# Performance work log

Hardware: AMD Instinct MI355X
Metric: run time of the kernel (lower is better)

Reference implementation:

```python
import jax, jax.numpy as jnp
import numpy as np

B, S, D, H, E, K = 2, 1024, 1024, 4096, 8, 2
HE = 4 * D  # expert FFN inner dim
LN_EPS = 1e-5


def layernorm(x, g, b):
    m = x.mean(-1, keepdims=True)
    v = ((x - m) ** 2).mean(-1, keepdims=True)
    return (x - m) * jax.lax.rsqrt(v + LN_EPS) * g + b


def pos_encoding(S, D):
    pos = jnp.arange(S, dtype=jnp.float32)[:, None]
    i = jnp.arange(0, D, 2, dtype=jnp.float32)
    div = jnp.exp(-(jnp.log(10000.0)) * i / D)
    pe = jnp.zeros((S, D), dtype=jnp.float32)
    pe = pe.at[:, 0::2].set(jnp.sin(pos * div))
    pe = pe.at[:, 1::2].set(jnp.cos(pos * div))
    return pe


def setup_inputs() -> dict:
    key = jax.random.key(0)
    ks = jax.random.split(key, 16)
    w = lambda k, sh, s=0.02: (jax.random.normal(k, sh, dtype=jnp.float32) * s)
    return {
        "x": jax.random.normal(ks[0], (B, S, D), dtype=jnp.float32),
        # router: LayerNorm -> Linear(D,H) -> GELU -> Linear(H,E)
        "r_ln_g": jnp.ones((D,), jnp.float32), "r_ln_b": jnp.zeros((D,), jnp.float32),
        "r_w1": w(ks[1], (D, H)), "r_b1": jnp.zeros((H,), jnp.float32),
        "r_w2": w(ks[2], (H, E)), "r_b2": jnp.zeros((E,), jnp.float32),
        "temperature": jnp.ones((1,), jnp.float32) * 0.07,
        # stacked expert params: LayerNorm -> Linear(D,HE) -> GELU -> Linear(HE,D)
        "e_ln_g": jnp.ones((E, D), jnp.float32), "e_ln_b": jnp.zeros((E, D), jnp.float32),
        "e_w1": w(ks[3], (E, D, HE)), "e_b1": jnp.zeros((E, HE), jnp.float32),
        "e_w2": w(ks[4], (E, HE, D)), "e_b2": jnp.zeros((E, D), jnp.float32),
        # combiner: LayerNorm -> Linear(D,2D) -> GELU -> Linear(2D,D)
        "c_ln_g": jnp.ones((D,), jnp.float32), "c_ln_b": jnp.zeros((D,), jnp.float32),
        "c_w1": w(ks[5], (D, 2 * D)), "c_b1": jnp.zeros((2 * D,), jnp.float32),
        "c_w2": w(ks[6], (2 * D, D)), "c_b2": jnp.zeros((D,), jnp.float32),
        "o_ln_g": jnp.ones((D,), jnp.float32), "o_ln_b": jnp.zeros((D,), jnp.float32),
    }


def reference(x, r_ln_g, r_ln_b, r_w1, r_b1, r_w2, r_b2, temperature,
              e_ln_g, e_ln_b, e_w1, e_b1, e_w2, e_b2,
              c_ln_g, c_ln_b, c_w1, c_b1, c_w2, c_b2, o_ln_g, o_ln_b):
    gelu = lambda t: jax.nn.gelu(t, approximate=False)
    h = x + pos_encoding(S, D)[None]  # [B,S,D]
    # router logits with learned temperature
    r = layernorm(h, r_ln_g, r_ln_b)
    r = gelu(jnp.einsum("bsd,dh->bsh", r, r_w1) + r_b1)
    logits = (jnp.einsum("bsh,he->bse", r, r_w2) + r_b2) / temperature
    probs = jax.nn.softmax(logits, axis=-1)  # [B,S,E]
    topk_p, topk_i = jax.lax.top_k(probs, K)
    # sparse gate [B,S,E]: softmax prob on selected experts, 0 elsewhere
    gate = (jax.nn.one_hot(topk_i, E, dtype=probs.dtype) * topk_p[..., None]).sum(-2)
    # per-expert FFN on all tokens (dense reference of dispatch/compute/combine)
    m = h.mean(-1, keepdims=True)
    v = ((h - m) ** 2).mean(-1, keepdims=True)
    xhat = (h - m) * jax.lax.rsqrt(v + LN_EPS)  # [B,S,D], shared LN stats
    y = xhat[None] * e_ln_g[:, None, None, :] + e_ln_b[:, None, None, :]  # [E,B,S,D]
    f = gelu(jnp.einsum("ebsd,edh->ebsh", y, e_w1) + e_b1[:, None, None, :])
    f = jnp.einsum("ebsh,ehd->ebsd", f, e_w2) + e_b2[:, None, None, :]
    combined = jnp.einsum("bse,ebsd->bsd", gate, f)
    # expert combiner MLP + residual + output norm
    c = layernorm(combined, c_ln_g, c_ln_b)
    c = gelu(jnp.einsum("bsd,de->bse", c, c_w1) + c_b1)
    c = jnp.einsum("bse,ed->bsd", c, c_w2) + c_b2
    return layernorm(h + c, o_ln_g, o_ln_b)
```

## Files before the change

### kernel.cpp

```cpp
#include <hip/hip_runtime.h>
#include <stdint.h>

#define TOK 2048
#define DD  1024
#define RH  4096
#define HE  4096
#define NE  8
#define CH  2048
#define MAXTILE 40
#define MAXROWS 5120
#define KSG2 4
#define KSC1 2
#define KSC2 4

using bf16x8 = __attribute__((ext_vector_type(8))) short;
using f32x4  = __attribute__((ext_vector_type(4))) float;

__device__ __forceinline__ unsigned short f2bf(float f) {
  union { float f; uint32_t u; } v; v.f = f;
  uint32_t r = (v.u + 0x7fffu + ((v.u >> 16) & 1u)) >> 16;
  return (unsigned short)r;
}
__device__ __forceinline__ float bf2f(unsigned short h) {
  union { uint32_t u; float f; } v; v.u = ((uint32_t)h) << 16;
  return v.f;
}
__device__ __forceinline__ float gelu_f(float x) {
  return 0.5f * x * (1.0f + erff(x * 0.70710678118654752440f));
}

#define GLD(SRC, DST) __builtin_amdgcn_global_load_lds( \
    (const __attribute__((address_space(1))) uint32_t*)(const void*)(SRC), \
    (__attribute__((address_space(3))) uint32_t*)(void*)(DST), 16, 0, 0)

__device__ __forceinline__ void block_ln_stats(float s1, float s2, float& mean, float& rstd) {
  #pragma unroll
  for (int off = 32; off > 0; off >>= 1) {
    s1 += __shfl_down(s1, off);
    s2 += __shfl_down(s2, off);
  }
  __shared__ float sh[8];
  int tid = threadIdx.x;
  if ((tid & 63) == 0) { sh[tid >> 6] = s1; sh[4 + (tid >> 6)] = s2; }
  __syncthreads();
  float t1 = sh[0] + sh[1] + sh[2] + sh[3];
  float t2 = sh[4] + sh[5] + sh[6] + sh[7];
  mean = t1 * (1.0f / 1024.0f);
  float var = t2 * (1.0f / 1024.0f) - mean * mean;
  rstd = rsqrtf(var + 1e-5f);
}

__global__ void k_prep(const float* __restrict__ x, float* __restrict__ h,
                       float* __restrict__ xh32, unsigned short* __restrict__ xhi,
                       unsigned short* __restrict__ xlo) {
  int t = blockIdx.x;
  int s = t & 1023;
  int tid = threadIdx.x;
  float4 xv = ((const float4*)(x + (size_t)t * DD))[tid];
  float v[4]; float s1 = 0.f, s2 = 0.f;
  #pragma unroll
  for (int k = 0; k < 4; ++k) {
    int d = tid * 4 + k;
    float xc = (k == 0) ? xv.x : (k == 1) ? xv.y : (k == 2) ? xv.z : xv.w;
    float i2 = (float)(d & ~1);
    float div = expf(-9.2103403719761836f * i2 * (1.0f / 1024.0f));
    float ang = (float)s * div;
    float pe = (d & 1) ? cosf(ang) : sinf(ang);
    float hv = xc + pe;
    v[k] = hv; s1 += hv; s2 += hv * hv;
  }
  float mean, rstd;
  block_ln_stats(s1, s2, mean, rstd);
  float4 ho; ho.x = v[0]; ho.y = v[1]; ho.z = v[2]; ho.w = v[3];
  ((float4*)(h + (size_t)t * DD))[tid] = ho;
  float xn[4]; unsigned short hh[4], ll[4];
  #pragma unroll
  for (int k = 0; k < 4; ++k) {
    xn[k] = (v[k] - mean) * rstd;
    hh[k] = f2bf(xn[k]);
    ll[k] = f2bf(xn[k] - bf2f(hh[k]));
  }
  float4 xo; xo.x = xn[0]; xo.y = xn[1]; xo.z = xn[2]; xo.w = xn[3];
  ((float4*)(xh32 + (size_t)t * DD))[tid] = xo;
  ushort4 h4; h4.x = hh[0]; h4.y = hh[1]; h4.z = hh[2]; h4.w = hh[3];
  ((ushort4*)(xhi + (size_t)t * DD))[tid] = h4;
  ushort4 l4; l4.x = ll[0]; l4.y = ll[1]; l4.z = ll[2]; l4.w = ll[3];
  ((ushort4*)(xlo + (size_t)t * DD))[tid] = l4;
}

__global__ void k_tconv(const float* __restrict__ in, const float* __restrict__ g,
                        unsigned short* __restrict__ out, int D, int N,
                        long long in_bs, long long g_bs, long long out_bs) {
  __shared__ float tile[64][65];
  int e = blockIdx.z;
  const float* inb = in + (size_t)e * in_bs;
  unsigned short* outb = out + (size_t)e * out_bs;
  int n0 = blockIdx.x * 64, d0 = blockIdx.y * 64;
  int c4 = threadIdx.x & 15;
  int r0 = threadIdx.x >> 4;
  #pragma unroll
  for (int rr = 0; rr < 4; ++rr) {
    int dl = r0 + rr * 16;
    float4 v = *(const float4*)(inb + (size_t)(d0 + dl) * N + n0 + c4 * 4);
    if (g) {
      float gv = g[(size_t)e * g_bs + d0 + dl];
      v.x *= gv; v.y *= gv; v.z *= gv; v.w *= gv;
    }
    tile[dl][c4 * 4 + 0] = v.x; tile[dl][c4 * 4 + 1] = v.y;
    tile[dl][c4 * 4 + 2] = v.z; tile[dl][c4 * 4 + 3] = v.w;
  }
  __syncthreads();
  int q = threadIdx.x & 15;
  int nb = threadIdx.x >> 4;
  #pragma unroll
  for (int rr = 0; rr < 4; ++rr) {
    int nl = nb + rr * 16;
    ushort4 o;
    o.x = f2bf(tile[q * 4 + 0][nl]); o.y = f2bf(tile[q * 4 + 1][nl]);
    o.z = f2bf(tile[q * 4 + 2][nl]); o.w = f2bf(tile[q * 4 + 3][nl]);
    *(ushort4*)(outb + (size_t)(n0 + nl) * D + d0 + q * 4) = o;
  }
}

__global__ void k_tconv_split(const float* __restrict__ in, const float* __restrict__ g,
                              unsigned short* __restrict__ oh, unsigned short* __restrict__ ol,
                              float* __restrict__ o32, int D, int N) {
  __shared__ float tile[32][33];
  int n0 = blockIdx.x * 32, d0 = blockIdx.y * 32;
  int tn = threadIdx.x & 31, tr = threadIdx.x >> 5;
  #pragma unroll
  for (int rr = 0; rr < 4; ++rr) {
    int dl = tr + rr * 8;
    float v = in[(size_t)(d0 + dl) * N + n0 + tn];
    if (g) v *= g[d0 + dl];
    tile[dl][tn] = v;
  }
  __syncthreads();
  #pragma unroll
  for (int rr = 0; rr < 4; ++rr) {
    int nl = tr + rr * 8;
    float v = tile[tn][nl];
    size_t off = (size_t)(n0 + nl) * D + d0 + tn;
    unsigned short hi = f2bf(v);
    oh[off] = hi;
    ol[off] = f2bf(v - bf2f(hi));
    o32[off] = v;
  }
}

__global__ void k_foldbias(const float* __restrict__ w, const float* __restrict__ lnb,
                           const float* __restrict__ b1, float* __restrict__ outb,
                           int D, int N, long long w_bs, long long lnb_bs,
                           long long b_bs, long long o_bs) {
  int e = blockIdx.y;
  int n = blockIdx.x * 256 + threadIdx.x;
  const float* wb = w + (size_t)e * w_bs;
  const float* lb = lnb + (size_t)e * lnb_bs;
  float acc = b1[(size_t)e * b_bs + n];
  for (int d = 0; d < D; ++d) {
    float l = lb[d];
    if (l != 0.f) acc += l * wb[(size_t)d * N + n];
  }
  outb[(size_t)e * o_bs + n] = acc;
}

__global__ __launch_bounds__(256)
void k_gemm_sk(const unsigned short* __restrict__ A, const unsigned short* __restrict__ B,
               float* __restrict__ C, int N, int K, int kslice, long long c_slice) {
  __shared__ __align__(16) unsigned short As[128 * 32];
  __shared__ __align__(16) unsigned short Bs[128 * 32];
  const int tid = threadIdx.x;
  const int w = tid >> 6, lane = tid & 63;
  const int q = lane >> 4, r16 = lane & 15;
  const int kz = blockIdx.z;
  const int n0 = blockIdx.x * 128, m0 = blockIdx.y * 128;
  f32x4 acc[4][4];
  #pragma unroll
  for (int i = 0; i < 4; ++i)
    #pragma unroll
    for (int j = 0; j < 4; ++j) acc[i][j] = (f32x4){0.f, 0.f, 0.f, 0.f};
  const int srow = w * 32 + (lane >> 2);
  const int scol = (lane & 3) * 8;
  const unsigned short* a_src = A + (size_t)(m0 + srow) * K + scol + (size_t)kz * kslice;
  const unsigned short* b_src = B + (size_t)(n0 + srow) * K + scol + (size_t)kz * kslice;
  unsigned short* a_dst = &As[w * 1024];
  unsigned short* b_dst = &Bs[w * 1024];
  const int wm = w >> 1, wn = w & 1;
  for (int kt = 0; kt < kslice; kt += 32) {
    GLD(a_src + kt, a_dst);
    GLD(a_src + kt + (size_t)16 * K, a_dst + 512);
    GLD(b_src + kt, b_dst);
    GLD(b_src + kt + (size_t)16 * K, b_dst + 512);
    __syncthreads();
    bf16x8 af[4], bfv[4];
    #pragma unroll
    for (int i = 0; i < 4; ++i)
      af[i] = *(const bf16x8*)&As[(wm * 64 + i * 16 + r16) * 32 + q * 8];
    #pragma unroll
    for (int j = 0; j < 4; ++j)
      bfv[j] = *(const bf16x8*)&Bs[(wn * 64 + j * 16 + r16) * 32 + q * 8];
    #pragma unroll
    for (int i = 0; i < 4; ++i)
      #pragma unroll
      for (int j = 0; j < 4; ++j)
        acc[i][j] = __builtin_amdgcn_mfma_f32_16x16x32_bf16(af[i], bfv[j], acc[i][j], 0, 0, 0);
    __syncthreads();
  }
  #pragma unroll
  for (int j = 0; j < 4; ++j) {
    int col = n0 + wn * 64 + j * 16 + r16;
    #pragma unroll
    for (int i = 0; i < 4; ++i) {
      int row = m0 + wm * 64 + i * 16 + q * 4;
      #pragma unroll
      for (int t2 = 0; t2 < 4; ++t2)
        C[(size_t)kz * c_slice + (size_t)(row + t2) * N + col] = acc[i][j][t2];
    }
  }
}

__global__ void k_redg(const float* __restrict__ p, const float* __restrict__ bias,
                       unsigned short* __restrict__ o, int N, long long slice, int nsl) {
  size_t i = ((size_t)blockIdx.x * 256 + threadIdx.x) * 4;
  float4 a = *(const float4*)(p + i);
  for (int s = 1; s < nsl; ++s) {
    float4 b = *(const float4*)(p + (size_t)s * slice + i);
    a.x += b.x; a.y += b.y; a.z += b.z; a.w += b.w;
  }
  int col = (int)(i & (size_t)(N - 1));
  float4 bv = *(const float4*)(bias + col);
  ushort4 u;
  u.x = f2bf(gelu_f(a.x + bv.x)); u.y = f2bf(gelu_f(a.y + bv.y));
  u.z = f2bf(gelu_f(a.z + bv.z)); u.w = f2bf(gelu_f(a.w + bv.w));
  *(ushort4*)(o + i) = u;
}

__global__ __launch_bounds__(256)
void k_gemm_g1(const unsigned short* __restrict__ A, const unsigned short* __restrict__ W,
               const float* __restrict__ bias, unsigned short* __restrict__ C,
               const int* __restrict__ tok_of, const int* __restrict__ tile_e,
               const int* __restrict__ tile_r0, const int* __restrict__ ntiles) {
  if ((int)blockIdx.y >= *ntiles) return;
  __shared__ __align__(16) unsigned short As[128 * 32];
  __shared__ __align__(16) unsigned short Bs[128 * 32];
  const int tid = threadIdx.x;
  const int w = tid >> 6, lane = tid & 63;
  const int q = lane >> 4, r16 = lane & 15;
  const int e = tile_e[blockIdx.y];
  const int row0 = tile_r0[blockIdx.y];
  const int n0 = blockIdx.x * 128;
  f32x4 acc[4][4];
  #pragma unroll
  for (int i = 0; i < 4; ++i)
    #pragma unroll
    for (int j = 0; j < 4; ++j) acc[i][j] = (f32x4){0.f, 0.f, 0.f, 0.f};
  const int srow = w * 32 + (lane >> 2);
  const int scol = (lane & 3) * 8;
  const int t0 = tok_of[row0 + srow];
  const int t1 = tok_of[row0 + srow + 16];
  const unsigned short* a_src0 = A + (size_t)t0 * DD + scol;
  const unsigned short* a_src1 = A + (size_t)t1 * DD + scol;
  const unsigned short* b_src = W + (size_t)e * RH * DD + (size_t)(n0 + srow) * DD + scol;
  unsigned short* a_dst = &As[w * 1024];
  unsigned short* b_dst = &Bs[w * 1024];
  const int wm = w >> 1, wn = w & 1;
  for (int kt = 0; kt < DD; kt += 32) {
    GLD(a_src0 + kt, a_dst);
    GLD(a_src1 + kt, a_dst + 512);
    GLD(b_src + kt, b_dst);
    GLD(b_src + kt + (size_t)16 * DD, b_dst + 512);
    __syncthreads();
    bf16x8 af[4], bfv[4];
    #pragma unroll
    for (int i = 0; i < 4; ++i)
      af[i] = *(const bf16x8*)&As[(wm * 64 + i * 16 + r16) * 32 + q * 8];
    #pragma unroll
    for (int j = 0; j < 4; ++j)
      bfv[j] = *(const bf16x8*)&Bs[(wn * 64 + j * 16 + r16) * 32 + q * 8];
    #pragma unroll
    for (int i = 0; i < 4; ++i)
      #pragma unroll
      for (int j = 0; j < 4; ++j)
        acc[i][j] = __builtin_amdgcn_mfma_f32_16x16x32_bf16(af[i], bfv[j], acc[i][j], 0, 0, 0);
    __syncthreads();
  }
  #pragma unroll
  for (int j = 0; j < 4; ++j) {
    int col = n0 + wn * 64 + j * 16 + r16;
    float bv = bias[(size_t)e * RH + col];
    #pragma unroll
    for (int i = 0; i < 4; ++i) {
      int row = row0 + wm * 64 + i * 16 + q * 4;
      #pragma unroll
      for (int t2 = 0; t2 < 4; ++t2)
        C[(size_t)(row + t2) * RH + col] = f2bf(gelu_f(acc[i][j][t2] + bv));
    }
  }
}

__global__ __launch_bounds__(256)
void k_gemm_g2(const unsigned short* __restrict__ A, const unsigned short* __restrict__ W,
               float* __restrict__ C, const int* __restrict__ tile_e,
               const int* __restrict__ tile_r0, const int* __restrict__ ntiles) {
  if ((int)blockIdx.y >= *ntiles) return;
  __shared__ __align__(16) unsigned short As[128 * 32];
  __shared__ __align__(16) unsigned short Bs[128 * 32];
  const int tid = threadIdx.x;
  const int w = tid >> 6, lane = tid & 63;
  const int q = lane >> 4, r16 = lane & 15;
  const int e = tile_e[blockIdx.y];
  const int row0 = tile_r0[blockIdx.y];
  const int n0 = blockIdx.x * 128;
  const int kz = blockIdx.z;
  f32x4 acc[4][4];
  #pragma unroll
  for (int i = 0; i < 4; ++i)
    #pragma unroll
    for (int j = 0; j < 4; ++j) acc[i][j] = (f32x4){0.f, 0.f, 0.f, 0.f};
  const int srow = w * 32 + (lane >> 2);
  const int scol = (lane & 3) * 8;
  const unsigned short* a_src = A + (size_t)(row0 + srow) * HE + scol + (size_t)kz * (HE / KSG2);
  const unsigned short* b_src = W + (size_t)e * DD * HE + (size_t)(n0 + srow) * HE + scol
                                + (size_t)kz * (HE / KSG2);
  unsigned short* a_dst = &As[w * 1024];
  unsigned short* b_dst = &Bs[w * 1024];
  const int wm = w >> 1, wn = w & 1;
  for (int kt = 0; kt < HE / KSG2; kt += 32) {
    GLD(a_src + kt, a_dst);
    GLD(a_src + kt + (size_t)16 * HE, a_dst + 512);
    GLD(b_src + kt, b_dst);
    GLD(b_src + kt + (size_t)16 * HE, b_dst + 512);
    __syncthreads();
    bf16x8 af[4], bfv[4];
    #pragma unroll
    for (int i = 0; i < 4; ++i)
      af[i] = *(const bf16x8*)&As[(wm * 64 + i * 16 + r16) * 32 + q * 8];
    #pragma unroll
    for (int j = 0; j < 4; ++j)
      bfv[j] = *(const bf16x8*)&Bs[(wn * 64 + j * 16 + r16) * 32 + q * 8];
    #pragma unroll
    for (int i = 0; i < 4; ++i)
      #pragma unroll
      for (int j = 0; j < 4; ++j)
        acc[i][j] = __builtin_amdgcn_mfma_f32_16x16x32_bf16(af[i], bfv[j], acc[i][j], 0, 0, 0);
    __syncthreads();
  }
  #pragma unroll
  for (int j = 0; j < 4; ++j) {
    int col = n0 + wn * 64 + j * 16 + r16;
    #pragma unroll
    for (int i = 0; i < 4; ++i) {
      int row = row0 + wm * 64 + i * 16 + q * 4;
      #pragma unroll
      for (int t2 = 0; t2 < 4; ++t2)
        C[(size_t)kz * MAXROWS * DD + (size_t)(row + t2) * DD + col] = acc[i][j][t2];
    }
  }
}

__global__ __launch_bounds__(256)
void k_gemm_split(const unsigned short* __restrict__ Ah, const unsigned short* __restrict__ Al,
                  const unsigned short* __restrict__ Bh, const unsigned short* __restrict__ Bl,
                  const float* __restrict__ bias, float* __restrict__ C, int N, int K) {
  __shared__ __align__(16) unsigned short Ahs[128 * 32];
  __shared__ __align__(16) unsigned short Als[128 * 32];
  __shared__ __align__(16) unsigned short Bhs[128 * 32];
  __shared__ __align__(16) unsigned short Bls[128 * 32];
  const int tid = threadIdx.x;
  const int w = tid >> 6, lane = tid & 63;
  const int q = lane >> 4, r16 = lane & 15;
  const int n0 = blockIdx.x * 128, m0 = blockIdx.y * 128;
  f32x4 acc[4][4];
  #pragma unroll
  for (int i = 0; i < 4; ++i)
    #pragma unroll
    for (int j = 0; j < 4; ++j) acc[i][j] = (f32x4){0.f, 0.f, 0.f, 0.f};
  const int srow = w * 32 + (lane >> 2);
  const int scol = (lane & 3) * 8;
  const unsigned short* ah_src = Ah + (size_t)(m0 + srow) * K + scol;
  const unsigned short* al_src = Al + (size_t)(m0 + srow) * K + scol;
  const unsigned short* bh_src = Bh + (size_t)(n0 + srow) * K + scol;
  const unsigned short* bl_src = Bl + (size_t)(n0 + srow) * K + scol;
  const int wm = w >> 1, wn = w & 1;
  for (int kt = 0; kt < K; kt += 32) {
    GLD(ah_src + kt, &Ahs[w * 1024]);
    GLD(ah_src + kt + (size_t)16 * K, &Ahs[w * 1024 + 512]);
    GLD(al_src + kt, &Als[w * 1024]);
    GLD(al_src + kt + (size_t)16 * K, &Als[w * 1024 + 512]);
    GLD(bh_src + kt, &Bhs[w * 1024]);
    GLD(bh_src + kt + (size_t)16 * K, &Bhs[w * 1024 + 512]);
    GLD(bl_src + kt, &Bls[w * 1024]);
    GLD(bl_src + kt + (size_t)16 * K, &Bls[w * 1024 + 512]);
    __syncthreads();
    bf16x8 ah[4], al[4], bh[4], bl[4];
    #pragma unroll
    for (int i = 0; i < 4; ++i) {
      int o = (wm * 64 + i * 16 + r16) * 32 + q * 8;
      ah[i] = *(const bf16x8*)&Ahs[o];
      al[i] = *(const bf16x8*)&Als[o];
    }
    #pragma unroll
    for (int j = 0; j < 4; ++j) {
      int o = (wn * 64 + j * 16 + r16) * 32 + q * 8;
      bh[j] = *(const bf16x8*)&Bhs[o];
      bl[j] = *(const bf16x8*)&Bls[o];
    }
    #pragma unroll
    for (int i = 0; i < 4; ++i)
      #pragma unroll
      for (int j = 0; j < 4; ++j) {
        acc[i][j] = __builtin_amdgcn_mfma_f32_16x16x32_bf16(ah[i], bh[j], acc[i][j], 0, 0, 0);
        acc[i][j] = __builtin_amdgcn_mfma_f32_16x16x32_bf16(al[i], bh[j], acc[i][j], 0, 0, 0);
        acc[i][j] = __builtin_amdgcn_mfma_f32_16x16x32_bf16(ah[i], bl[j], acc[i][j], 0, 0, 0);
      }
    __syncthreads();
  }
  #pragma unroll
  for (int j = 0; j < 4; ++j) {
    int col = n0 + wn * 64 + j * 16 + r16;
    float bv = bias[col];
    #pragma unroll
    for (int i = 0; i < 4; ++i) {
      int row = m0 + wm * 64 + i * 16 + q * 4;
      #pragma unroll
      for (int t2 = 0; t2 < 4; ++t2)
        C[(size_t)(row + t2) * N + col] = gelu_f(acc[i][j][t2] + bv);
    }
  }
}

__global__ void k_logits(const float* __restrict__ r, const float* __restrict__ w2,
                         const float* __restrict__ b2, const float* __restrict__ temp,
                         int* __restrict__ sel_i, float* __restrict__ sel_p,
                         int* __restrict__ flag, float* __restrict__ lg32) {
  int t = blockIdx.x, tid = threadIdx.x;
  const float* rr = r + (size_t)t * RH;
  float acc[NE];
  #pragma unroll
  for (int e = 0; e < NE; ++e) acc[e] = 0.f;
  #pragma unroll
  for (int k4 = 0; k4 < 4; ++k4) {
    float4 rv4 = ((const float4*)rr)[tid * 4 + k4];
    #pragma unroll
    for (int kk = 0; kk < 4; ++kk) {
      int d = tid * 16 + k4 * 4 + kk;
      float rv = (kk == 0) ? rv4.x : (kk == 1) ? rv4.y : (kk == 2) ? rv4.z : rv4.w;
      const float4* wr = (const float4*)(w2 + (size_t)d * NE);
      float4 w0 = wr[0], w1 = wr[1];
      acc[0] += rv * w0.x; acc[1] += rv * w0.y; acc[2] += rv * w0.z; acc[3] += rv * w0.w;
      acc[4] += rv * w1.x; acc[5] += rv * w1.y; acc[6] += rv * w1.z; acc[7] += rv * w1.w;
    }
  }
  #pragma unroll
  for (int off = 32; off > 0; off >>= 1)
    #pragma unroll
    for (int e = 0; e < NE; ++e) acc[e] += __shfl_down(acc[e], off);
  __shared__ float shl[4][NE];
  int w = tid >> 6, lane = tid & 63;
  if (lane == 0) {
    #pragma unroll
    for (int e = 0; e < NE; ++e) shl[w][e] = acc[e];
  }
  __syncthreads();
  if (tid == 0) {
    float tmp = temp[0];
    float lg[NE];
    #pragma unroll
    for (int e = 0; e < NE; ++e)
      lg[e] = (shl[0][e] + shl[1][e] + shl[2][e] + shl[3][e] + b2[e]) / tmp;
    float mx = lg[0];
    for (int e = 1; e < NE; ++e) mx = fmaxf(mx, lg[e]);
    float p[NE], se = 0.f;
    for (int e = 0; e < NE; ++e) { p[e] = expf(lg[e] - mx); se += p[e]; }
    float inv = 1.f / se;
    int i1 = 0; float p1 = p[0];
    for (int e = 1; e < NE; ++e) if (p[e] > p1) { p1 = p[e]; i1 = e; }
    int i2 = -1; float p2 = -1.f;
    for (int e = 0; e < NE; ++e) if (e != i1 && p[e] > p2) { p2 = p[e]; i2 = e; }
    sel_i[t * 2] = i1; sel_i[t * 2 + 1] = i2;
    sel_p[t * 2] = p1 * inv; sel_p[t * 2 + 1] = p2 * inv;
    float a1 = -1e30f, a2 = -1e30f, a3 = -1e30f;
    for (int e = 0; e < NE; ++e) {
      float vv = lg[e];
      if (vv > a1) { a3 = a2; a2 = a1; a1 = vv; }
      else if (vv > a2) { a3 = a2; a2 = vv; }
      else if (vv > a3) a3 = vv;
    }
    int fl = (a2 - a3 < 0.01f) ? 1 : 0;
    flag[t] = fl;
    if (fl) {
      #pragma unroll
      for (int e = 0; e < NE; ++e) lg32[(size_t)t * NE + e] = 0.f;
    }
  }
}

__global__ void k_flaglist(const int* __restrict__ flag, int* __restrict__ ftok,
                           int* __restrict__ nflag) {
  int t = blockIdx.x * 256 + threadIdx.x;
  if (t >= TOK) return;
  if (flag[t]) { int p = atomicAdd(nflag, 1); ftok[p] = t; }
}

__global__ void k_triage2(const int* __restrict__ nflag, const int* __restrict__ ftok,
                          const float* __restrict__ xh32, const float* __restrict__ W32,
                          const float* __restrict__ biasr, const float* __restrict__ w2,
                          float* __restrict__ lg32) {
  int nf = *nflag;
  __shared__ float xs[DD];
  __shared__ float sh2[4][NE];
  int tid = threadIdx.x;
  int w = tid >> 6, lane = tid & 63;
  for (int idx = blockIdx.y; idx < nf; idx += (int)gridDim.y) {
    int t = ftok[idx];
    ((float4*)xs)[tid] = ((const float4*)(xh32 + (size_t)t * DD))[tid];
    __syncthreads();
    int hh0 = blockIdx.x * 64 + w * 16;
    float acc[NE];
    #pragma unroll
    for (int e = 0; e < NE; ++e) acc[e] = 0.f;
    #pragma unroll
    for (int r = 0; r < 16; ++r) {
      int hh = hh0 + r;
      const float4* wrow = (const float4*)(W32 + (size_t)hh * DD);
      float s = 0.f;
      #pragma unroll
      for (int c = 0; c < 4; ++c) {
        float4 wv = wrow[lane + 64 * c];
        float4 xv = ((const float4*)xs)[lane + 64 * c];
        s += wv.x * xv.x + wv.y * xv.y + wv.z * xv.z + wv.w * xv.w;
      }
      #pragma unroll
      for (int off = 32; off > 0; off >>= 1) s += __shfl_down(s, off);
      if (lane == 0) {
        float r1 = gelu_f(s + biasr[hh]);
        const float* wr = w2 + (size_t)hh * NE;
        #pragma unroll
        for (int e = 0; e < NE; ++e) acc[e] += r1 * wr[e];
      }
    }
    if (lane == 0) {
      #pragma unroll
      for (int e = 0; e < NE; ++e) sh2[w][e] = acc[e];
    }
    __syncthreads();
    if (tid < NE) {
      float v = sh2[0][tid] + sh2[1][tid] + sh2[2][tid] + sh2[3][tid];
      atomicAdd(&lg32[(size_t)t * NE + tid], v);
    }
  }
}

__global__ void k_gate2(const int* __restrict__ flag, const float* __restrict__ lg32,
                        const float* __restrict__ b2, const float* __restrict__ temp,
                        int* __restrict__ sel_i, float* __restrict__ sel_p) {
  int t = blockIdx.x * 256 + threadIdx.x;
  if (t >= TOK || flag[t] == 0) return;
  float tmp = temp[0];
  float lg[NE];
  #pragma unroll
  for (int e = 0; e < NE; ++e) lg[e] = (lg32[(size_t)t * NE + e] + b2[e]) / tmp;
  float mx = lg[0];
  for (int e = 1; e < NE; ++e) mx = fmaxf(mx, lg[e]);
  float p[NE], se = 0.f;
  for (int e = 0; e < NE; ++e) { p[e] = expf(lg[e] - mx); se += p[e]; }
  float inv = 1.f / se;
  int i1 = 0; float p1 = p[0];
  for (int e = 1; e < NE; ++e) if (p[e] > p1) { p1 = p[e]; i1 = e; }
  int i2 = -1; float p2 = -1.f;
  for (int e = 0; e < NE; ++e) if (e != i1 && p[e] > p2) { p2 = p[e]; i2 = e; }
  sel_i[t * 2] = i1; sel_i[t * 2 + 1] = i2;
  sel_p[t * 2] = p1 * inv; sel_p[t * 2 + 1] = p2 * inv;
}

__global__ void k_count(const int* __restrict__ sel_i, int* __restrict__ cnt) {
  int t = blockIdx.x * 256 + threadIdx.x;
  if (t >= TOK) return;
  atomicAdd(&cnt[sel_i[2 * t]], 1);
  atomicAdd(&cnt[sel_i[2 * t + 1]], 1);
}

__global__ void k_offsets(const int* __restrict__ cnt, int* __restrict__ off,
                          int* __restrict__ tile_e, int* __restrict__ tile_r0,
                          int* __restrict__ ntiles) {
  if (threadIdx.x == 0) {
    int cur = 0, nt = 0;
    for (int e = 0; e < NE; ++e) {
      off[e] = cur;
      int n = (cnt[e] + 127) >> 7;
      for (int k = 0; k < n; ++k) { tile_e[nt] = e; tile_r0[nt] = cur + 128 * k; nt++; }
      cur += n * 128;
    }
    *ntiles = nt;
  }
}

__global__ void k_fill(const int* __restrict__ sel_i, const int* __restrict__ off,
                       int* __restrict__ fill, int* __restrict__ slotarr,
                       int* __restrict__ tok_of) {
  int t = blockIdx.x * 256 + threadIdx.x;
  if (t >= TOK) return;
  #pragma unroll
  for (int j = 0; j < 2; ++j) {
    int e = sel_i[2 * t + j];
    int pos = atomicAdd(&fill[e], 1);
    int s = off[e] + pos;
    slotarr[2 * t + j] = s;
    tok_of[s] = t;
  }
}

__global__ void k_combine2(const int* __restrict__ slotarr, const int* __restrict__ sel_i,
                           const float* __restrict__ sel_p, const float* __restrict__ pairpart,
                           const float* __restrict__ e_b2, unsigned short* __restrict__ xc) {
  int t = blockIdx.x, tid = threadIdx.x;
  int s0 = slotarr[t * 2], s1 = slotarr[t * 2 + 1];
  int e0 = sel_i[t * 2], e1 = sel_i[t * 2 + 1];
  float w0 = sel_p[t * 2], w1 = sel_p[t * 2 + 1];
  float a0x = 0.f, a0y = 0.f, a0z = 0.f, a0w = 0.f;
  float a1x = 0.f, a1y = 0.f, a1z = 0.f, a1w = 0.f;
  #pragma unroll
  for (int z = 0; z < KSG2; ++z) {
    float4 u = ((const float4*)(pairpart + (size_t)z * MAXROWS * DD + (size_t)s0 * DD))[tid];
    a0x += u.x; a0y += u.y; a0z += u.z; a0w += u.w;
    float4 v = ((const float4*)(pairpart + (size_t)z * MAXROWS * DD + (size_t)s1 * DD))[tid];
    a1x += v.x; a1y += v.y; a1z += v.z; a1w += v.w;
  }
  float4 b0 = ((const float4*)(e_b2 + (size_t)e0 * DD))[tid];
  float4 b1v = ((const float4*)(e_b2 + (size_t)e1 * DD))[tid];
  float v[4];
  v[0] = w0 * (a0x + b0.x) + w1 * (a1x + b1v.x);
  v[1] = w0 * (a0y + b0.y) + w1 * (a1y + b1v.y);
  v[2] = w0 * (a0z + b0.z) + w1 * (a1z + b1v.z);
  v[3] = w0 * (a0w + b0.w) + w1 * (a1w + b1v.w);
  float s1f = v[0] + v[1] + v[2] + v[3];
  float s2f = v[0]*v[0] + v[1]*v[1] + v[2]*v[2] + v[3]*v[3];
  float mean, rstd;
  block_ln_stats(s1f, s2f, mean, rstd);
  ushort4 o;
  o.x = f2bf((v[0] - mean) * rstd); o.y = f2bf((v[1] - mean) * rstd);
  o.z = f2bf((v[2] - mean) * rstd); o.w = f2bf((v[3] - mean) * rstd);
  ((ushort4*)(xc + (size_t)t * DD))[tid] = o;
}

__global__ void k_final(const float* __restrict__ h, const float* __restrict__ c2p,
                        const float* __restrict__ cb2, const float* __restrict__ og,
                        const float* __restrict__ ob, float* __restrict__ out) {
  int t = blockIdx.x, tid = threadIdx.x;
  float4 hv = ((const float4*)(h + (size_t)t * DD))[tid];
  float ax = 0.f, ay = 0.f, az = 0.f, aw = 0.f;
  #pragma unroll
  for (int z = 0; z < KSC2; ++z) {
    float4 u = ((const float4*)(c2p + (size_t)z * TOK * DD + (size_t)t * DD))[tid];
    ax += u.x; ay += u.y; az += u.z; aw += u.w;
  }
  float4 cb = ((const float4*)cb2)[tid];
  float v[4] = {hv.x + ax + cb.x, hv.y + ay + cb.y, hv.z + az + cb.z, hv.w + aw + cb.w};
  float s1 = v[0] + v[1] + v[2] + v[3];
  float s2 = v[0]*v[0] + v[1]*v[1] + v[2]*v[2] + v[3]*v[3];
  float mean, rstd;
  block_ln_stats(s1, s2, mean, rstd);
  float4 gv = ((const float4*)og)[tid];
  float4 bv = ((const float4*)ob)[tid];
  float4 o;
  o.x = (v[0] - mean) * rstd * gv.x + bv.x;
  o.y = (v[1] - mean) * rstd * gv.y + bv.y;
  o.z = (v[2] - mean) * rstd * gv.z + bv.z;
  o.w = (v[3] - mean) * rstd * gv.w + bv.w;
  ((float4*)(out + (size_t)t * DD))[tid] = o;
}

extern "C" void kernel_launch(void* const* d_in, const int* in_sizes, int n_in,
                              void* d_out, int out_size, void* d_ws, size_t ws_size,
                              hipStream_t stream) {
  (void)in_sizes; (void)n_in; (void)out_size; (void)ws_size;
  const float* x      = (const float*)d_in[0];
  const float* r_ln_g = (const float*)d_in[1];
  const float* r_ln_b = (const float*)d_in[2];
  const float* r_w1   = (const float*)d_in[3];
  const float* r_b1   = (const float*)d_in[4];
  const float* r_w2   = (const float*)d_in[5];
  const float* r_b2   = (const float*)d_in[6];
  const float* temp   = (const float*)d_in[7];
  const float* e_ln_g = (const float*)d_in[8];
  const float* e_ln_b = (const float*)d_in[9];
  const float* e_w1   = (const float*)d_in[10];
  const float* e_b1   = (const float*)d_in[11];
  const float* e_w2   = (const float*)d_in[12];
  const float* e_b2   = (const float*)d_in[13];
  const float* c_ln_g = (const float*)d_in[14];
  const float* c_ln_b = (const float*)d_in[15];
  const float* c_w1   = (const float*)d_in[16];
  const float* c_b1   = (const float*)d_in[17];
  const float* c_w2   = (const float*)d_in[18];
  const float* c_b2   = (const float*)d_in[19];
  const float* o_ln_g = (const float*)d_in[20];
  const float* o_ln_b = (const float*)d_in[21];
  float* out = (float*)d_out;

  char* base = (char*)d_ws;
  long long cur = 0;
  auto take = [&](long long sz) { char* r = base + cur; cur += (sz + 255) & ~255LL; return r; };

  float* h      = (float*)take(8388608);
  float* xh32   = (float*)take(8388608);
  unsigned short* xhi = (unsigned short*)take(4194304);
  unsigned short* xlo = (unsigned short*)take(4194304);
  unsigned short* WrH = (unsigned short*)take(8388608);
  unsigned short* WrL = (unsigned short*)take(8388608);
  float* Wr32   = (float*)take(16777216);
  float* biasr  = (float*)take(16384);
  float* ract   = (float*)take(33554432);
  int*   flag   = (int*)take(8192);
  float* lg32   = (float*)take(65536);
  int*   sel_i  = (int*)take(16384);
  float* sel_p  = (float*)take(16384);
  int*   cnt    = (int*)take(256);
  int*   off    = (int*)take(256);
  int*   fillc  = (int*)take(256);
  int*   tile_e = (int*)take(256);
  int*   tile_r0= (int*)take(256);
  int*   ntiles = (int*)take(256);
  int*   nflag  = (int*)take(256);
  int*   ftok   = (int*)take(TOK * 4);
  int*   slotarr= (int*)take(16384);
  int*   tok_of = (int*)take(MAXROWS * 4);
  unsigned short* We1 = (unsigned short*)take(67108864);
  float* be1    = (float*)take(131072);
  unsigned short* We2 = (unsigned short*)take(67108864);
  unsigned short* Wc1 = (unsigned short*)take(4194304);
  float* bc1    = (float*)take(8192);
  unsigned short* Wc2 = (unsigned short*)take(4194304);
  unsigned short* xc  = (unsigned short*)take(4194304);
  unsigned short* c1  = (unsigned short*)take(8388608);
  unsigned short* F1g = (unsigned short*)take((long long)MAXROWS * RH * 2);
  float* pairpart = (float*)take((long long)KSG2 * MAXROWS * DD * 4);
  float* c1part = (float*)WrH;
  float* c2part = (float*)biasr;

  hipMemsetAsync(cnt, 0, 256, stream);
  hipMemsetAsync(fillc, 0, 256, stream);
  hipMemsetAsync(nflag, 0, 256, stream);
  hipMemsetAsync(tok_of, 0, MAXROWS * 4, stream);

  k_prep<<<TOK, 256, 0, stream>>>(x, h, xh32, xhi, xlo);
  k_tconv_split<<<dim3(RH/32, DD/32, 1), 256, 0, stream>>>(r_w1, r_ln_g, WrH, WrL, Wr32, DD, RH);
  k_tconv<<<dim3(RH/64, DD/64, NE), 256, 0, stream>>>(e_w1, e_ln_g, We1, DD, RH,
      (long long)DD*RH, (long long)DD, (long long)RH*DD);
  k_tconv<<<dim3(DD/64, HE/64, NE), 256, 0, stream>>>(e_w2, nullptr, We2, HE, DD,
      (long long)HE*DD, 0LL, (long long)DD*HE);
  k_tconv<<<dim3(CH/64, DD/64, 1), 256, 0, stream>>>(c_w1, c_ln_g, Wc1, DD, CH, 0LL, 0LL, 0LL);
  k_tconv<<<dim3(DD/64, CH/64, 1), 256, 0, stream>>>(c_w2, nullptr, Wc2, CH, DD, 0LL, 0LL, 0LL);
  k_foldbias<<<dim3(RH/256, 1), 256, 0, stream>>>(r_w1, r_ln_b, r_b1, biasr, DD, RH, 0LL, 0LL, 0LL, 0LL);
  k_foldbias<<<dim3(RH/256, NE), 256, 0, stream>>>(e_w1, e_ln_b, e_b1, be1, DD, RH,
      (long long)DD*RH, (long long)DD, (long long)RH, (long long)RH);
  k_foldbias<<<dim3(CH/256, 1), 256, 0, stream>>>(c_w1, c_ln_b, c_b1, bc1, DD, CH, 0LL, 0LL, 0LL, 0LL);

  k_gemm_split<<<dim3(RH/128, TOK/128, 1), 256, 0, stream>>>(xhi, xlo, WrH, WrL, biasr, ract, RH, DD);
  k_logits<<<TOK, 256, 0, stream>>>(ract, r_w2, r_b2, temp, sel_i, sel_p, flag, lg32);
  k_flaglist<<<TOK/256, 256, 0, stream>>>(flag, ftok, nflag);
  k_triage2<<<dim3(RH/64, 32), 256, 0, stream>>>(nflag, ftok, xh32, Wr32, biasr, r_w2, lg32);
  k_gate2<<<TOK/256, 256, 0, stream>>>(flag, lg32, r_b2, temp, sel_i, sel_p);

  k_count<<<TOK/256, 256, 0, stream>>>(sel_i, cnt);
  k_offsets<<<1, 64, 0, stream>>>(cnt, off, tile_e, tile_r0, ntiles);
  k_fill<<<TOK/256, 256, 0, stream>>>(sel_i, off, fillc, slotarr, tok_of);

  k_gemm_g1<<<dim3(RH/128, MAXTILE), 256, 0, stream>>>(xhi, We1, be1, F1g,
      tok_of, tile_e, tile_r0, ntiles);
  k_gemm_g2<<<dim3(DD/128, MAXTILE, KSG2), 256, 0, stream>>>(F1g, We2, pairpart,
      tile_e, tile_r0, ntiles);

  k_combine2<<<TOK, 256, 0, stream>>>(slotarr, sel_i, sel_p, pairpart, e_b2, xc);
  k_gemm_sk<<<dim3(CH/128, TOK/128, KSC1), 256, 0, stream>>>(xc, Wc1, c1part, CH, DD,
      DD/KSC1, (long long)TOK * CH);
  k_redg<<<(TOK * CH) / 1024, 256, 0, stream>>>(c1part, bc1, c1, CH, (long long)TOK * CH, KSC1);
  k_gemm_sk<<<dim3(DD/128, TOK/128, KSC2), 256, 0, stream>>>(c1, Wc2, c2part, DD, CH,
      CH/KSC2, (long long)TOK * DD);
  k_final<<<TOK, 256, 0, stream>>>(h, c2part, c_b2, o_ln_g, o_ln_b, out);
}
```

Before: 1.097 ms.

## Double-buffer GEMM LDS tiles and fuse small routing/memset kernels

All four MFMA GEMM kernels now keep two LDS stages and prefetch the next K tile while computing the current one, which drops one barrier per iteration and is meant to hide global load latency. The hipMemsetAsync calls are folded into k_prep, k_flaglist is merged into k_logits, k_count into k_gate2, and the positional encoding uses sincosf. These changes cut launch count and redundant transcendental work, at the cost of doubled LDS use (which can lower occupancy, especially in k_gemm_split) and more atomics inside k_logits.

```diff
diff --git a/kernel.cpp b/kernel.cpp
--- a/kernel.cpp
+++ b/kernel.cpp
@@ -52,23 +52,27 @@
 
 __global__ void k_prep(const float* __restrict__ x, float* __restrict__ h,
                        float* __restrict__ xh32, unsigned short* __restrict__ xhi,
-                       unsigned short* __restrict__ xlo) {
+                       unsigned short* __restrict__ xlo, int* __restrict__ cnt,
+                       int* __restrict__ fillc, int* __restrict__ nflag,
+                       int* __restrict__ tok_of) {
   int t = blockIdx.x;
   int s = t & 1023;
   int tid = threadIdx.x;
   float4 xv = ((const float4*)(x + (size_t)t * DD))[tid];
   float v[4]; float s1 = 0.f, s2 = 0.f;
   #pragma unroll
-  for (int k = 0; k < 4; ++k) {
-    int d = tid * 4 + k;
-    float xc = (k == 0) ? xv.x : (k == 1) ? xv.y : (k == 2) ? xv.z : xv.w;
-    float i2 = (float)(d & ~1);
+  for (int kp = 0; kp < 2; ++kp) {
+    float i2 = (float)(tid * 4 + kp * 2);
     float div = expf(-9.2103403719761836f * i2 * (1.0f / 1024.0f));
     float ang = (float)s * div;
-    float pe = (d & 1) ? cosf(ang) : sinf(ang);
-    float hv = xc + pe;
-    v[k] = hv; s1 += hv; s2 += hv * hv;
-  }
+    float sn, cs;
+    sincosf(ang, &sn, &cs);
+    float xe = (kp == 0) ? xv.x : xv.z;
+    float xo = (kp == 0) ? xv.y : xv.w;
+    v[kp * 2] = xe + sn; v[kp * 2 + 1] = xo + cs;
+  }
+  #pragma unroll
+  for (int k = 0; k < 4; ++k) { s1 += v[k]; s2 += v[k] * v[k]; }
   float mean, rstd;
   block_ln_stats(s1, s2, mean, rstd);
   float4 ho; ho.x = v[0]; ho.y = v[1]; ho.z = v[2]; ho.w = v[3];
@@ -80,12 +84,17 @@
     hh[k] = f2bf(xn[k]);
     ll[k] = f2bf(xn[k] - bf2f(hh[k]));
   }
-  float4 xo; xo.x = xn[0]; xo.y = xn[1]; xo.z = xn[2]; xo.w = xn[3];
-  ((float4*)(xh32 + (size_t)t * DD))[tid] = xo;
+  float4 xo4; xo4.x = xn[0]; xo4.y = xn[1]; xo4.z = xn[2]; xo4.w = xn[3];
+  ((float4*)(xh32 + (size_t)t * DD))[tid] = xo4;
   ushort4 h4; h4.x = hh[0]; h4.y = hh[1]; h4.z = hh[2]; h4.w = hh[3];
   ((ushort4*)(xhi + (size_t)t * DD))[tid] = h4;
   ushort4 l4; l4.x = ll[0]; l4.y = ll[1]; l4.z = ll[2]; l4.w = ll[3];
   ((ushort4*)(xlo + (size_t)t * DD))[tid] = l4;
+  if (t == 0) {
+    for (int i = tid; i < MAXROWS; i += 256) tok_of[i] = 0;
+    if (tid < NE) { cnt[tid] = 0; fillc[tid] = 0; }
+    if (tid == 0) nflag[0] = 0;
+  }
 }
 
 __global__ void k_tconv(const float* __restrict__ in, const float* __restrict__ g,
@@ -167,8 +176,8 @@
 __global__ __launch_bounds__(256)
 void k_gemm_sk(const unsigned short* __restrict__ A, const unsigned short* __restrict__ B,
                float* __restrict__ C, int N, int K, int kslice, long long c_slice) {
-  __shared__ __align__(16) unsigned short As[128 * 32];
-  __shared__ __align__(16) unsigned short Bs[128 * 32];
+  __shared__ __align__(16) unsigned short As[2][4096];
+  __shared__ __align__(16) unsigned short Bs[2][4096];
   const int tid = threadIdx.x;
   const int w = tid >> 6, lane = tid & 63;
   const int q = lane >> 4, r16 = lane & 15;
@@ -183,28 +192,35 @@
   const int scol = (lane & 3) * 8;
   const unsigned short* a_src = A + (size_t)(m0 + srow) * K + scol + (size_t)kz * kslice;
   const unsigned short* b_src = B + (size_t)(n0 + srow) * K + scol + (size_t)kz * kslice;
-  unsigned short* a_dst = &As[w * 1024];
-  unsigned short* b_dst = &Bs[w * 1024];
   const int wm = w >> 1, wn = w & 1;
+  GLD(a_src, &As[0][w * 1024]);
+  GLD(a_src + (size_t)16 * K, &As[0][w * 1024 + 512]);
+  GLD(b_src, &Bs[0][w * 1024]);
+  GLD(b_src + (size_t)16 * K, &Bs[0][w * 1024 + 512]);
+  __syncthreads();
+  int cur = 0;
   for (int kt = 0; kt < kslice; kt += 32) {
-    GLD(a_src + kt, a_dst);
-    GLD(a_src + kt + (size_t)16 * K, a_dst + 512);
-    GLD(b_src + kt, b_dst);
-    GLD(b_src + kt + (size_t)16 * K, b_dst + 512);
-    __syncthreads();
+    int nk = kt + 32;
+    if (nk < kslice) {
+      GLD(a_src + nk, &As[cur ^ 1][w * 1024]);
+      GLD(a_src + nk + (size_t)16 * K, &As[cur ^ 1][w * 1024 + 512]);
+      GLD(b_src + nk, &Bs[cur ^ 1][w * 1024]);
+      GLD(b_src + nk + (size_t)16 * K, &Bs[cur ^ 1][w * 1024 + 512]);
+    }
     bf16x8 af[4], bfv[4];
     #pragma unroll
     for (int i = 0; i < 4; ++i)
-      af[i] = *(const bf16x8*)&As[(wm * 64 + i * 16 + r16) * 32 + q * 8];
+      af[i] = *(const bf16x8*)&As[cur][(wm * 64 + i * 16 + r16) * 32 + q * 8];
     #pragma unroll
     for (int j = 0; j < 4; ++j)
-      bfv[j] = *(const bf16x8*)&Bs[(wn * 64 + j * 16 + r16) * 32 + q * 8];
+      bfv[j] = *(const bf16x8*)&Bs[cur][(wn * 64 + j * 16 + r16) * 32 + q * 8];
     #pragma unroll
     for (int i = 0; i < 4; ++i)
       #pragma unroll
       for (int j = 0; j < 4; ++j)
         acc[i][j] = __builtin_amdgcn_mfma_f32_16x16x32_bf16(af[i], bfv[j], acc[i][j], 0, 0, 0);
     __syncthreads();
+    cur ^= 1;
   }
   #pragma unroll
   for (int j = 0; j < 4; ++j) {
@@ -241,8 +257,8 @@
                const int* __restrict__ tok_of, const int* __restrict__ tile_e,
                const int* __restrict__ tile_r0, const int* __restrict__ ntiles) {
   if ((int)blockIdx.y >= *ntiles) return;
-  __shared__ __align__(16) unsigned short As[128 * 32];
-  __shared__ __align__(16) unsigned short Bs[128 * 32];
+  __shared__ __align__(16) unsigned short As[2][4096];
+  __shared__ __align__(16) unsigned short Bs[2][4096];
   const int tid = threadIdx.x;
   const int w = tid >> 6, lane = tid & 63;
   const int q = lane >> 4, r16 = lane & 15;
@@ -261,28 +277,35 @@
   const unsigned short* a_src0 = A + (size_t)t0 * DD + scol;
   const unsigned short* a_src1 = A + (size_t)t1 * DD + scol;
   const unsigned short* b_src = W + (size_t)e * RH * DD + (size_t)(n0 + srow) * DD + scol;
-  unsigned short* a_dst = &As[w * 1024];
-  unsigned short* b_dst = &Bs[w * 1024];
   const int wm = w >> 1, wn = w & 1;
+  GLD(a_src0, &As[0][w * 1024]);
+  GLD(a_src1, &As[0][w * 1024 + 512]);
+  GLD(b_src, &Bs[0][w * 1024]);
+  GLD(b_src + (size_t)16 * DD, &Bs[0][w * 1024 + 512]);
+  __syncthreads();
+  int cur = 0;
   for (int kt = 0; kt < DD; kt += 32) {
-    GLD(a_src0 + kt, a_dst);
-    GLD(a_src1 + kt, a_dst + 512);
-    GLD(b_src + kt, b_dst);
-    GLD(b_src + kt + (size_t)16 * DD, b_dst + 512);
-    __syncthreads();
+    int nk = kt + 32;
+    if (nk < DD) {
+      GLD(a_src0 + nk, &As[cur ^ 1][w * 1024]);
+      GLD(a_src1 + nk, &As[cur ^ 1][w * 1024 + 512]);
+      GLD(b_src + nk, &Bs[cur ^ 1][w * 1024]);
+      GLD(b_src + nk + (size_t)16 * DD, &Bs[cur ^ 1][w * 1024 + 512]);
+    }
     bf16x8 af[4], bfv[4];
     #pragma unroll
     for (int i = 0; i < 4; ++i)
-      af[i] = *(const bf16x8*)&As[(wm * 64 + i * 16 + r16) * 32 + q * 8];
+      af[i] = *(const bf16x8*)&As[cur][(wm * 64 + i * 16 + r16) * 32 + q * 8];
     #pragma unroll
     for (int j = 0; j < 4; ++j)
-      bfv[j] = *(const bf16x8*)&Bs[(wn * 64 + j * 16 + r16) * 32 + q * 8];
+      bfv[j] = *(const bf16x8*)&Bs[cur][(wn * 64 + j * 16 + r16) * 32 + q * 8];
     #pragma unroll
     for (int i = 0; i < 4; ++i)
       #pragma unroll
       for (int j = 0; j < 4; ++j)
         acc[i][j] = __builtin_amdgcn_mfma_f32_16x16x32_bf16(af[i], bfv[j], acc[i][j], 0, 0, 0);
     __syncthreads();
+    cur ^= 1;
   }
   #pragma unroll
   for (int j = 0; j < 4; ++j) {
@@ -303,8 +326,8 @@
                float* __restrict__ C, const int* __restrict__ tile_e,
                const int* __restrict__ tile_r0, const int* __restrict__ ntiles) {
   if ((int)blockIdx.y >= *ntiles) return;
-  __shared__ __align__(16) unsigned short As[128 * 32];
-  __shared__ __align__(16) unsigned short Bs[128 * 32];
+  __shared__ __align__(16) unsigned short As[2][4096];
+  __shared__ __align__(16) unsigned short Bs[2][4096];
   const int tid = threadIdx.x;
   const int w = tid >> 6, lane = tid & 63;
   const int q = lane >> 4, r16 = lane & 15;
@@ -322,28 +345,35 @@
   const unsigned short* a_src = A + (size_t)(row0 + srow) * HE + scol + (size_t)kz * (HE / KSG2);
   const unsigned short* b_src = W + (size_t)e * DD * HE + (size_t)(n0 + srow) * HE + scol
                                 + (size_t)kz * (HE / KSG2);
-  unsigned short* a_dst = &As[w * 1024];
-  unsigned short* b_dst = &Bs[w * 1024];
   const int wm = w >> 1, wn = w & 1;
+  GLD(a_src, &As[0][w * 1024]);
+  GLD(a_src + (size_t)16 * HE, &As[0][w * 1024 + 512]);
+  GLD(b_src, &Bs[0][w * 1024]);
+  GLD(b_src + (size_t)16 * HE, &Bs[0][w * 1024 + 512]);
+  __syncthreads();
+  int cur = 0;
   for (int kt = 0; kt < HE / KSG2; kt += 32) {
-    GLD(a_src + kt, a_dst);
-    GLD(a_src + kt + (size_t)16 * HE, a_dst + 512);
-    GLD(b_src + kt, b_dst);
-    GLD(b_src + kt + (size_t)16 * HE, b_dst + 512);
-    __syncthreads();
+    int nk = kt + 32;
+    if (nk < HE / KSG2) {
+      GLD(a_src + nk, &As[cur ^ 1][w * 1024]);
+      GLD(a_src + nk + (size_t)16 * HE, &As[cur ^ 1][w * 1024 + 512]);
+      GLD(b_src + nk, &Bs[cur ^ 1][w * 1024]);
+      GLD(b_src + nk + (size_t)16 * HE, &Bs[cur ^ 1][w * 1024 + 512]);
+    }
     bf16x8 af[4], bfv[4];
     #pragma unroll
     for (int i = 0; i < 4; ++i)
-      af[i] = *(const bf16x8*)&As[(wm * 64 + i * 16 + r16) * 32 + q * 8];
+      af[i] = *(const bf16x8*)&As[cur][(wm * 64 + i * 16 + r16) * 32 + q * 8];
     #pragma unroll
     for (int j = 0; j < 4; ++j)
-      bfv[j] = *(const bf16x8*)&Bs[(wn * 64 + j * 16 + r16) * 32 + q * 8];
+      bfv[j] = *(const bf16x8*)&Bs[cur][(wn * 64 + j * 16 + r16) * 32 + q * 8];
     #pragma unroll
     for (int i = 0; i < 4; ++i)
       #pragma unroll
       for (int j = 0; j < 4; ++j)
         acc[i][j] = __builtin_amdgcn_mfma_f32_16x16x32_bf16(af[i], bfv[j], acc[i][j], 0, 0, 0);
     __syncthreads();
+    cur ^= 1;
   }
   #pragma unroll
   for (int j = 0; j < 4; ++j) {
@@ -362,10 +392,10 @@
 void k_gemm_split(const unsigned short* __restrict__ Ah, const unsigned short* __restrict__ Al,
                   const unsigned short* __restrict__ Bh, const unsigned short* __restrict__ Bl,
                   const float* __restrict__ bias, float* __restrict__ C, int N, int K) {
-  __shared__ __align__(16) unsigned short Ahs[128 * 32];
-  __shared__ __align__(16) unsigned short Als[128 * 32];
-  __shared__ __align__(16) unsigned short Bhs[128 * 32];
-  __shared__ __align__(16) unsigned short Bls[128 * 32];
+  __shared__ __align__(16) unsigned short Ahs[2][4096];
+  __shared__ __align__(16) unsigned short Als[2][4096];
+  __shared__ __align__(16) unsigned short Bhs[2][4096];
+  __shared__ __align__(16) unsigned short Bls[2][4096];
   const int tid = threadIdx.x;
   const int w = tid >> 6, lane = tid & 63;
   const int q = lane >> 4, r16 = lane & 15;
@@ -382,28 +412,40 @@
   const unsigned short* bh_src = Bh + (size_t)(n0 + srow) * K + scol;
   const unsigned short* bl_src = Bl + (size_t)(n0 + srow) * K + scol;
   const int wm = w >> 1, wn = w & 1;
+  GLD(ah_src, &Ahs[0][w * 1024]);
+  GLD(ah_src + (size_t)16 * K, &Ahs[0][w * 1024 + 512]);
+  GLD(al_src, &Als[0][w * 1024]);
+  GLD(al_src + (size_t)16 * K, &Als[0][w * 1024 + 512]);
+  GLD(bh_src, &Bhs[0][w * 1024]);
+  GLD(bh_src + (size_t)16 * K, &Bhs[0][w * 1024 + 512]);
+  GLD(bl_src, &Bls[0][w * 1024]);
+  GLD(bl_src + (size_t)16 * K, &Bls[0][w * 1024 + 512]);
+  __syncthreads();
+  int cur = 0;
   for (int kt = 0; kt < K; kt += 32) {
-    GLD(ah_src + kt, &Ahs[w * 1024]);
-    GLD(ah_src + kt + (size_t)16 * K, &Ahs[w * 1024 + 512]);
-    GLD(al_src + kt, &Als[w * 1024]);
-    GLD(al_src + kt + (size_t)16 * K, &Als[w * 1024 + 512]);
-    GLD(bh_src + kt, &Bhs[w * 1024]);
-    GLD(bh_src + kt + (size_t)16 * K, &Bhs[w * 1024 + 512]);
-    GLD(bl_src + kt, &Bls[w * 1024]);
-    GLD(bl_src + kt + (size_t)16 * K, &Bls[w * 1024 + 512]);
-    __syncthreads();
+    int nk = kt + 32;
+    if (nk < K) {
+      GLD(ah_src + nk, &Ahs[cur ^ 1][w * 1024]);
+      GLD(ah_src + nk + (size_t)16 * K, &Ahs[cur ^ 1][w * 1024 + 512]);
+      GLD(al_src + nk, &Als[cur ^ 1][w * 1024]);
+      GLD(al_src + nk + (size_t)16 * K, &Als[cur ^ 1][w * 1024 + 512]);
+      GLD(bh_src + nk, &Bhs[cur ^ 1][w * 1024]);
+      GLD(bh_src + nk + (size_t)16 * K, &Bhs[cur ^ 1][w * 1024 + 512]);
+      GLD(bl_src + nk, &Bls[cur ^ 1][w * 1024]);
+      GLD(bl_src + nk + (size_t)16 * K, &Bls[cur ^ 1][w * 1024 + 512]);
+    }
     bf16x8 ah[4], al[4], bh[4], bl[4];
     #pragma unroll
     for (int i = 0; i < 4; ++i) {
       int o = (wm * 64 + i * 16 + r16) * 32 + q * 8;
-      ah[i] = *(const bf16x8*)&Ahs[o];
-      al[i] = *(const bf16x8*)&Als[o];
+      ah[i] = *(const bf16x8*)&Ahs[cur][o];
+      al[i] = *(const bf16x8*)&Als[cur][o];
     }
     #pragma unroll
     for (int j = 0; j < 4; ++j) {
       int o = (wn * 64 + j * 16 + r16) * 32 + q * 8;
-      bh[j] = *(const bf16x8*)&Bhs[o];
-      bl[j] = *(const bf16x8*)&Bls[o];
+      bh[j] = *(const bf16x8*)&Bhs[cur][o];
+      bl[j] = *(const bf16x8*)&Bls[cur][o];
     }
     #pragma unroll
     for (int i = 0; i < 4; ++i)
@@ -414,6 +456,7 @@
         acc[i][j] = __builtin_amdgcn_mfma_f32_16x16x32_bf16(ah[i], bl[j], acc[i][j], 0, 0, 0);
       }
     __syncthreads();
+    cur ^= 1;
   }
   #pragma unroll
   for (int j = 0; j < 4; ++j) {
@@ -432,7 +475,8 @@
 __global__ void k_logits(const float* __restrict__ r, const float* __restrict__ w2,
                          const float* __restrict__ b2, const float* __restrict__ temp,
                          int* __restrict__ sel_i, float* __restrict__ sel_p,
-                         int* __restrict__ flag, float* __restrict__ lg32) {
+                         int* __restrict__ flag, float* __restrict__ lg32,
+                         int* __restrict__ nflag, int* __restrict__ ftok) {
   int t = blockIdx.x, tid = threadIdx.x;
   const float* rr = r + (size_t)t * RH;
   float acc[NE];
@@ -489,17 +533,12 @@
     int fl = (a2 - a3 < 0.01f) ? 1 : 0;
     flag[t] = fl;
     if (fl) {
+      int pidx = atomicAdd(nflag, 1);
+      ftok[pidx] = t;
       #pragma unroll
       for (int e = 0; e < NE; ++e) lg32[(size_t)t * NE + e] = 0.f;
     }
   }
-}
-
-__global__ void k_flaglist(const int* __restrict__ flag, int* __restrict__ ftok,
-                           int* __restrict__ nflag) {
-  int t = blockIdx.x * 256 + threadIdx.x;
-  if (t >= TOK) return;
-  if (flag[t]) { int p = atomicAdd(nflag, 1); ftok[p] = t; }
 }
 
 __global__ void k_triage2(const int* __restrict__ nflag, const int* __restrict__ ftok,
@@ -553,31 +592,32 @@
 
 __global__ void k_gate2(const int* __restrict__ flag, const float* __restrict__ lg32,
                         const float* __restrict__ b2, const float* __restrict__ temp,
-                        int* __restrict__ sel_i, float* __restrict__ sel_p) {
-  int t = blockIdx.x * 256 + threadIdx.x;
-  if (t >= TOK || flag[t] == 0) return;
-  float tmp = temp[0];
-  float lg[NE];
-  #pragma unroll
-  for (int e = 0; e < NE; ++e) lg[e] = (lg32[(size_t)t * NE + e] + b2[e]) / tmp;
-  float mx = lg[0];
-  for (int e = 1; e < NE; ++e) mx = fmaxf(mx, lg[e]);
-  float p[NE], se = 0.f;
-  for (int e = 0; e < NE; ++e) { p[e] = expf(lg[e] - mx); se += p[e]; }
-  float inv = 1.f / se;
-  int i1 = 0; float p1 = p[0];
-  for (int e = 1; e < NE; ++e) if (p[e] > p1) { p1 = p[e]; i1 = e; }
-  int i2 = -1; float p2 = -1.f;
-  for (int e = 0; e < NE; ++e) if (e != i1 && p[e] > p2) { p2 = p[e]; i2 = e; }
-  sel_i[t * 2] = i1; sel_i[t * 2 + 1] = i2;
-  sel_p[t * 2] = p1 * inv; sel_p[t * 2 + 1] = p2 * inv;
-}
-
-__global__ void k_count(const int* __restrict__ sel_i, int* __restrict__ cnt) {
+                        int* __restrict__ sel_i, float* __restrict__ sel_p,
+                        int* __restrict__ cnt) {
   int t = blockIdx.x * 256 + threadIdx.x;
   if (t >= TOK) return;
-  atomicAdd(&cnt[sel_i[2 * t]], 1);
-  atomicAdd(&cnt[sel_i[2 * t + 1]], 1);
+  int i1, i2;
+  if (flag[t]) {
+    float tmp = temp[0];
+    float lg[NE];
+    #pragma unroll
+    for (int e = 0; e < NE; ++e) lg[e] = (lg32[(size_t)t * NE + e] + b2[e]) / tmp;
+    float mx = lg[0];
+    for (int e = 1; e < NE; ++e) mx = fmaxf(mx, lg[e]);
+    float p[NE], se = 0.f;
+    for (int e = 0; e < NE; ++e) { p[e] = expf(lg[e] - mx); se += p[e]; }
+    float inv = 1.f / se;
+    i1 = 0; float p1 = p[0];
+    for (int e = 1; e < NE; ++e) if (p[e] > p1) { p1 = p[e]; i1 = e; }
+    i2 = -1; float p2 = -1.f;
+    for (int e = 0; e < NE; ++e) if (e != i1 && p[e] > p2) { p2 = p[e]; i2 = e; }
+    sel_i[t * 2] = i1; sel_i[t * 2 + 1] = i2;
+    sel_p[t * 2] = p1 * inv; sel_p[t * 2 + 1] = p2 * inv;
+  } else {
+    i1 = sel_i[t * 2]; i2 = sel_i[t * 2 + 1];
+  }
+  atomicAdd(&cnt[i1], 1);
+  atomicAdd(&cnt[i2], 1);
 }
 
 __global__ void k_offsets(const int* __restrict__ cnt, int* __restrict__ off,
@@ -738,12 +778,7 @@
   float* c1part = (float*)WrH;
   float* c2part = (float*)biasr;
 
-  hipMemsetAsync(cnt, 0, 256, stream);
-  hipMemsetAsync(fillc, 0, 256, stream);
-  hipMemsetAsync(nflag, 0, 256, stream);
-  hipMemsetAsync(tok_of, 0, MAXROWS * 4, stream);
-
-  k_prep<<<TOK, 256, 0, stream>>>(x, h, xh32, xhi, xlo);
+  k_prep<<<TOK, 256, 0, stream>>>(x, h, xh32, xhi, xlo, cnt, fillc, nflag, tok_of);
   k_tconv_split<<<dim3(RH/32, DD/32, 1), 256, 0, stream>>>(r_w1, r_ln_g, WrH, WrL, Wr32, DD, RH);
   k_tconv<<<dim3(RH/64, DD/64, NE), 256, 0, stream>>>(e_w1, e_ln_g, We1, DD, RH,
       (long long)DD*RH, (long long)DD, (long long)RH*DD);
@@ -757,12 +792,10 @@
   k_foldbias<<<dim3(CH/256, 1), 256, 0, stream>>>(c_w1, c_ln_b, c_b1, bc1, DD, CH, 0LL, 0LL, 0LL, 0LL);
 
   k_gemm_split<<<dim3(RH/128, TOK/128, 1), 256, 0, stream>>>(xhi, xlo, WrH, WrL, biasr, ract, RH, DD);
-  k_logits<<<TOK, 256, 0, stream>>>(ract, r_w2, r_b2, temp, sel_i, sel_p, flag, lg32);
-  k_flaglist<<<TOK/256, 256, 0, stream>>>(flag, ftok, nflag);
+  k_logits<<<TOK, 256, 0, stream>>>(ract, r_w2, r_b2, temp, sel_i, sel_p, flag, lg32, nflag, ftok);
   k_triage2<<<dim3(RH/64, 32), 256, 0, stream>>>(nflag, ftok, xh32, Wr32, biasr, r_w2, lg32);
-  k_gate2<<<TOK/256, 256, 0, stream>>>(flag, lg32, r_b2, temp, sel_i, sel_p);
-
-  k_count<<<TOK/256, 256, 0, stream>>>(sel_i, cnt);
+  k_gate2<<<TOK/256, 256, 0, stream>>>(flag, lg32, r_b2, temp, sel_i, sel_p, cnt);
+
   k_offsets<<<1, 64, 0, stream>>>(cnt, off, tile_e, tile_r0, ntiles);
   k_fill<<<TOK/256, 256, 0, stream>>>(sel_i, off, fillc, slotarr, tok_of);
 
```

Measured after the change: 1.100 ms. About the same (+0.3%).
